# Kernel optimization log

Measured on AMD Instinct MI355X. Metric: run time of the kernel, lower is better.

The kernel has to match this reference:

```python
import jax, jax.numpy as jnp
import numpy as np

B, S, E = 2, 4096, 512

def setup_inputs() -> dict:
    key = jax.random.key(0)
    kx, kq, kk, kv, ko = jax.random.split(key, 5)
    scale = 1.0 / np.sqrt(E)  # init-style scaling for weights
    return {
        "x": jax.random.normal(kx, (B, S, E), dtype=jnp.float32),
        "Wq": jax.random.normal(kq, (E, E), dtype=jnp.float32) * scale,
        "Wk": jax.random.normal(kk, (E, E), dtype=jnp.float32) * scale,
        "Wv": jax.random.normal(kv, (E, E), dtype=jnp.float32) * scale,
        "Wo": jax.random.normal(ko, (E, E), dtype=jnp.float32) * scale,
        "bo": jnp.zeros((E,), dtype=jnp.float32),
    }

def reference(x, Wq, Wk, Wv, Wo, bo):
    # nn.Linear: y = x @ W.T  (weights stored [out, in])
    q = jnp.einsum("bse,fe->bsf", x, Wq)
    k = jnp.einsum("bse,fe->bsf", x, Wk)
    v = jnp.einsum("bse,fe->bsf", x, Wv)
    inv_scale = 1.0 / jnp.sqrt(jnp.asarray(x.shape[-1], x.dtype))
    scores = jnp.einsum("bqe,bke->bqk", q, k) * inv_scale  # [B,S,S]
    S_len = x.shape[1]
    # torch.triu(ones) keeps j >= i; masked_fill where triu==0 masks j < i
    row = jnp.arange(S_len)[:, None]
    col = jnp.arange(S_len)[None, :]
    keep = col >= row  # [S,S], faithfully anti-causal as in the source
    scores = jnp.where(keep[None, :, :], scores, jnp.asarray(-jnp.inf, scores.dtype))
    attn = jax.nn.softmax(scores, axis=-1)
    # dropout p=0.0 -> identity
    out = jnp.einsum("bqk,bke->bqe", attn, v)
    return jnp.einsum("bse,fe->bsf", out, Wo) + bo
```

## Files before the change

kernel.cpp:

```cpp
#include <hip/hip_runtime.h>
#include <hip/hip_bf16.h>

#define S_LEN 4096
#define E_DIM 512
#define B_DIM 2
#define M_ROWS (B_DIM * S_LEN)

typedef __attribute__((ext_vector_type(8))) short short8;
typedef __attribute__((ext_vector_type(4))) float floatx4;

__device__ __forceinline__ unsigned short f2bf(float f) {
    unsigned u = __float_as_uint(f);
    unsigned r = (u + 0x7fffu + ((u >> 16) & 1u)) >> 16;
    return (unsigned short)r;
}
__device__ __forceinline__ float bf2f(unsigned short u) {
    return __uint_as_float((unsigned)u << 16);
}

__device__ __forceinline__ void async_copy16(unsigned short* lds, const unsigned short* g) {
    auto gp = (const __attribute__((address_space(1))) unsigned int*)g;
    auto lp = (__attribute__((address_space(3))) unsigned int*)lds;
    __builtin_amdgcn_global_load_lds(gp, lp, 16, 0, 0);
}

struct MapArg { unsigned short m[576]; };

__global__ __launch_bounds__(256) void convert_bf16(
    const float* __restrict__ x,  const float* __restrict__ wq,
    const float* __restrict__ wk, const float* __restrict__ wv,
    const float* __restrict__ wo, unsigned short* __restrict__ dstU,
    unsigned short* __restrict__ dstWo)
{
    long i = (long)blockIdx.x * 1024 + (long)threadIdx.x * 4;
    const float* src; long off; unsigned short* dst; long doff;
    if      (i < 4194304) { src = x;  off = i;           dst = dstU;  doff = i; }
    else if (i < 4456448) { src = wq; off = i - 4194304; dst = dstU;  doff = i; }
    else if (i < 4718592) { src = wk; off = i - 4456448; dst = dstU;  doff = i; }
    else if (i < 4980736) { src = wv; off = i - 4718592; dst = dstU;  doff = i; }
    else                  { src = wo; off = i - 4980736; dst = dstWo; doff = i - 4980736; }
    float4 v = *(const float4*)(src + off);
    ushort4 o;
    o.x = f2bf(v.x); o.y = f2bf(v.y); o.z = f2bf(v.z); o.w = f2bf(v.w);
    *(ushort4*)(dst + doff) = o;
}

__device__ __forceinline__ void gemm_core(
    const unsigned short* __restrict__ A, const unsigned short* __restrict__ W,
    void* __restrict__ Cv, const float* __restrict__ bias, int mode,
    int m0, int n0)
{
    __shared__ unsigned short As[128 * 32];
    __shared__ unsigned short Bs[128 * 32];
    const int tid = threadIdx.x;
    const int lane = tid & 63, wave = tid >> 6;
    const int wm = wave >> 1, wn = wave & 1;
    const int q4 = lane >> 4, l16 = lane & 15;

    floatx4 acc[4][4];
#pragma unroll
    for (int i = 0; i < 4; ++i)
#pragma unroll
        for (int j = 0; j < 4; ++j) acc[i][j] = (floatx4){0.f, 0.f, 0.f, 0.f};

    const int srow = lane >> 2;
    const int scol = (lane & 3) * 8;

    for (int k0 = 0; k0 < 512; k0 += 32) {
        async_copy16(&As[(wave * 16) * 32],
                     A + (size_t)(m0 + wave * 16 + srow) * 512 + k0 + scol);
        async_copy16(&As[(64 + wave * 16) * 32],
                     A + (size_t)(m0 + 64 + wave * 16 + srow) * 512 + k0 + scol);
        async_copy16(&Bs[(wave * 16) * 32],
                     W + (size_t)(n0 + wave * 16 + srow) * 512 + k0 + scol);
        async_copy16(&Bs[(64 + wave * 16) * 32],
                     W + (size_t)(n0 + 64 + wave * 16 + srow) * 512 + k0 + scol);
        __syncthreads();
        short8 af[4], bfr[4];
#pragma unroll
        for (int i = 0; i < 4; ++i) {
            af[i]  = *(const short8*)&As[(wm * 64 + i * 16 + l16) * 32 + q4 * 8];
            bfr[i] = *(const short8*)&Bs[(wn * 64 + i * 16 + l16) * 32 + q4 * 8];
        }
#pragma unroll
        for (int i = 0; i < 4; ++i)
#pragma unroll
            for (int j = 0; j < 4; ++j)
                acc[i][j] = __builtin_amdgcn_mfma_f32_16x16x32_bf16(af[i], bfr[j], acc[i][j], 0, 0, 0);
        __syncthreads();
    }

    if (mode == 0) {
        unsigned short* C = (unsigned short*)Cv;
#pragma unroll
        for (int i = 0; i < 4; ++i) {
            int rowb = m0 + wm * 64 + i * 16 + q4 * 4;
#pragma unroll
            for (int j = 0; j < 4; ++j) {
                int col = n0 + wn * 64 + j * 16 + l16;
#pragma unroll
                for (int rg = 0; rg < 4; ++rg)
                    C[(size_t)(rowb + rg) * 512 + col] = f2bf(acc[i][j][rg]);
            }
        }
    } else if (mode == 1) {
        unsigned short* C = (unsigned short*)Cv;
#pragma unroll
        for (int i = 0; i < 4; ++i) {
            int grow = m0 + wm * 64 + i * 16 + q4 * 4;
            int b = grow >> 12, s = grow & 4095;
#pragma unroll
            for (int j = 0; j < 4; ++j) {
                int e = n0 + wn * 64 + j * 16 + l16;
                ushort4 pk;
                pk.x = f2bf(acc[i][j][0]); pk.y = f2bf(acc[i][j][1]);
                pk.z = f2bf(acc[i][j][2]); pk.w = f2bf(acc[i][j][3]);
                *(ushort4*)(C + (size_t)b * 512 * 4096 + (size_t)e * 4096 + s) = pk;
            }
        }
    } else {
        float* C = (float*)Cv;
#pragma unroll
        for (int i = 0; i < 4; ++i) {
            int rowb = m0 + wm * 64 + i * 16 + q4 * 4;
#pragma unroll
            for (int j = 0; j < 4; ++j) {
                int col = n0 + wn * 64 + j * 16 + l16;
                float bv = bias[col];
#pragma unroll
                for (int rg = 0; rg < 4; ++rg)
                    C[(size_t)(rowb + rg) * 512 + col] = acc[i][j][rg] + bv;
            }
        }
    }
}

__global__ __launch_bounds__(256) void gemm_qkv(
    const unsigned short* __restrict__ xb,
    const unsigned short* __restrict__ Wqb, const unsigned short* __restrict__ Wkb,
    const unsigned short* __restrict__ Wvb,
    unsigned short* __restrict__ Qb, unsigned short* __restrict__ Kb,
    unsigned short* __restrict__ Vtb)
{
    const int z = blockIdx.z;
    const unsigned short* W = (z == 0) ? Wqb : (z == 1) ? Wkb : Wvb;
    unsigned short* C = (z == 0) ? Qb : (z == 1) ? Kb : Vtb;
    gemm_core(xb, W, C, nullptr, (z == 2) ? 1 : 0, blockIdx.y * 128, blockIdx.x * 128);
}

__global__ __launch_bounds__(256) void gemm_out(
    const unsigned short* __restrict__ AOb, const unsigned short* __restrict__ Wob,
    const float* __restrict__ bo, float* __restrict__ out)
{
    gemm_core(AOb, Wob, out, bo, 2, blockIdx.y * 128, blockIdx.x * 128);
}

__global__ __launch_bounds__(512, 2) void flash_mfma(
    const unsigned short* __restrict__ Qg, const unsigned short* __restrict__ Kg,
    const unsigned short* __restrict__ Vt,
    unsigned short* __restrict__ Oh, float* __restrict__ Lb, MapArg map)
{
    const int enc = map.m[blockIdx.x];
    const int tile = enc & 63, ch = (enc >> 6) & 7, bb = enc >> 9;
    const int i0 = tile * 64;
    const int lo0 = 512 * ch, hi = lo0 + 512;
    const int lo = (i0 > lo0) ? i0 : lo0;

    const int tid = threadIdx.x;
    const int lane = tid & 63, w = tid >> 6;
    const int s = w & 3, h = w >> 2;
    const int q4 = lane >> 4, l16 = lane & 15;
    const float scale = 0.044194173824159216f;
    const float MREF = 4.0f;

    __shared__ float Sred[4][64][36];
    __shared__ unsigned short Plds[64][40];
    __shared__ float Lred[64][8];

    const size_t rowbase = (size_t)bb * S_LEN;
    const size_t vbase   = (size_t)bb * 512 * 4096;

    short8 aq[4][4];
#pragma unroll
    for (int mg = 0; mg < 4; ++mg)
#pragma unroll
        for (int ks = 0; ks < 4; ++ks)
            aq[mg][ks] = *(const short8*)(Qg + (rowbase + i0 + mg * 16 + l16) * 512
                                          + s * 128 + ks * 32 + q4 * 8);

    floatx4 oacc[4][4];
#pragma unroll
    for (int mg = 0; mg < 4; ++mg)
#pragma unroll
        for (int nc = 0; nc < 4; ++nc) oacc[mg][nc] = (floatx4){0.f, 0.f, 0.f, 0.f};

    const int r = tid >> 3;
    const int g = tid & 7;
    float l_acc = 0.f;

    auto step = [&](int j0, short8 (&bkc)[4], short8 (&bkn)[4], int jn) {
        short8 vf[4];
#pragma unroll
        for (int nc = 0; nc < 4; ++nc)
            vf[nc] = *(const short8*)(Vt + vbase
                + (size_t)(w * 64 + nc * 16 + l16) * 4096 + j0 + q4 * 8);
#pragma unroll
        for (int ks = 0; ks < 4; ++ks)
            bkn[ks] = *(const short8*)(Kg + (rowbase + jn + h * 16 + l16) * 512
                                       + s * 128 + ks * 32 + q4 * 8);
        floatx4 sf[4];
#pragma unroll
        for (int mg = 0; mg < 4; ++mg) sf[mg] = (floatx4){0.f, 0.f, 0.f, 0.f};
        __builtin_amdgcn_s_setprio(1);
#pragma unroll
        for (int ks = 0; ks < 4; ++ks)
#pragma unroll
            for (int mg = 0; mg < 4; ++mg)
                sf[mg] = __builtin_amdgcn_mfma_f32_16x16x32_bf16(
                    bkc[ks], aq[mg][ks], sf[mg], 0, 0, 0);
        __builtin_amdgcn_s_setprio(0);
#pragma unroll
        for (int mg = 0; mg < 4; ++mg)
            *(floatx4*)&Sred[s][mg * 16 + l16][h * 16 + q4 * 4] = sf[mg];
        __syncthreads();

        float4 a0 = *(const float4*)&Sred[0][r][4 * g];
        float4 a1 = *(const float4*)&Sred[1][r][4 * g];
        float4 a2 = *(const float4*)&Sred[2][r][4 * g];
        float4 a3 = *(const float4*)&Sred[3][r][4 * g];
        float sv[4] = { a0.x + a1.x + a2.x + a3.x, a0.y + a1.y + a2.y + a3.y,
                        a0.z + a1.z + a2.z + a3.z, a0.w + a1.w + a2.w + a3.w };
        ushort4 pk;
        float p0, p1, p2, p3;
        {
            int key = j0 + 4 * g;
            int row = i0 + r;
            p0 = (key + 0 >= row) ? __expf(sv[0] * scale - MREF) : 0.f;
            p1 = (key + 1 >= row) ? __expf(sv[1] * scale - MREF) : 0.f;
            p2 = (key + 2 >= row) ? __expf(sv[2] * scale - MREF) : 0.f;
            p3 = (key + 3 >= row) ? __expf(sv[3] * scale - MREF) : 0.f;
        }
        l_acc += p0 + p1 + p2 + p3;
        pk.x = f2bf(p0); pk.y = f2bf(p1); pk.z = f2bf(p2); pk.w = f2bf(p3);
        *(ushort4*)&Plds[r][4 * g] = pk;
        __syncthreads();

        short8 ap[4];
#pragma unroll
        for (int mg = 0; mg < 4; ++mg)
            ap[mg] = *(const short8*)&Plds[mg * 16 + l16][q4 * 8];
        __builtin_amdgcn_s_setprio(1);
#pragma unroll
        for (int mg = 0; mg < 4; ++mg)
#pragma unroll
            for (int nc = 0; nc < 4; ++nc)
                oacc[mg][nc] = __builtin_amdgcn_mfma_f32_16x16x32_bf16(
                    ap[mg], vf[nc], oacc[mg][nc], 0, 0, 0);
        __builtin_amdgcn_s_setprio(0);
    };

    short8 bkA[4], bkB[4];
    int j0 = hi - 32;
#pragma unroll
    for (int ks = 0; ks < 4; ++ks)
        bkA[ks] = *(const short8*)(Kg + (rowbase + j0 + h * 16 + l16) * 512
                                   + s * 128 + ks * 32 + q4 * 8);
    while (j0 >= lo) {
        int jn = (j0 - 32 >= lo) ? j0 - 32 : lo;
        step(j0, bkA, bkB, jn);
        j0 -= 32;
        if (j0 < lo) break;
        jn = (j0 - 32 >= lo) ? j0 - 32 : lo;
        step(j0, bkB, bkA, jn);
        j0 -= 32;
    }
    __syncthreads();

    const int slot = 8 * ch * (ch + 1) + bb * 8 * (ch + 1) + tile;

    Lred[r][g] = l_acc;
    __syncthreads();
    if (tid < 64) {
        float sum = 0.f;
#pragma unroll
        for (int gg = 0; gg < 8; ++gg) sum += Lred[tid][gg];
        Lb[(size_t)slot * 64 + tid] = sum;
    }

    unsigned short* Op = Oh + (size_t)slot * 64 * 512;
#pragma unroll
    for (int mg = 0; mg < 4; ++mg)
#pragma unroll
        for (int nc = 0; nc < 4; ++nc)
#pragma unroll
            for (int rg = 0; rg < 4; ++rg)
                Op[(size_t)(mg * 16 + q4 * 4 + rg) * 512 + w * 64 + nc * 16 + l16]
                    = f2bf(oacc[mg][nc][rg]);
}

__global__ __launch_bounds__(256) void flash_merge(
    const unsigned short* __restrict__ Oh, const float* __restrict__ Lb,
    unsigned short* __restrict__ AO)
{
    const int row = blockIdx.x;
    const int c = threadIdx.x * 2;
    const int bb = row >> 12, i = row & 4095;
    const int t = i >> 6, ri = i & 63;
    const int chmin = i >> 9;
    float lsum = 0.f, v0 = 0.f, v1 = 0.f;
    for (int ch = chmin; ch < 8; ++ch) {
        int slot = 8 * ch * (ch + 1) + bb * 8 * (ch + 1) + t;
        lsum += Lb[(size_t)slot * 64 + ri];
        const unsigned short* p = Oh + (size_t)slot * 64 * 512 + (size_t)ri * 512 + c;
        v0 += bf2f(p[0]);
        v1 += bf2f(p[1]);
    }
    float inv = 1.f / lsum;
    ushort2 o; o.x = f2bf(v0 * inv); o.y = f2bf(v1 * inv);
    *(ushort2*)(AO + (size_t)row * 512 + c) = o;
}

static MapArg build_map() {
    int enc[576], steps[576], n = 0;
    for (int bb = 0; bb < 2; ++bb)
        for (int ch = 0; ch < 8; ++ch)
            for (int t = 0; t < 8 * (ch + 1); ++t) {
                int i0 = t * 64, lo0 = 512 * ch, hi = lo0 + 512;
                int lo = (i0 > lo0) ? i0 : lo0;
                enc[n] = t | (ch << 6) | (bb << 9);
                steps[n] = (hi - lo) / 32;
                ++n;
            }
    static int buck[9][576];
    int bn[9] = {0};
    for (int i = 0; i < n; ++i) { int b = steps[i] >> 1; buck[b][bn[b]++] = enc[i]; }
    MapArg mp{};
    int a = 0;
    for (int c = 0; c < 16; ++c) {
        mp.m[c] = (unsigned short)buck[8][a++];
        mp.m[256 + c] = (unsigned short)buck[8][a++];
        mp.m[512 + c] = (unsigned short)buck[1][c];
    }
    for (int c = 16; c < 32; ++c) {
        mp.m[c] = (unsigned short)buck[8][a++];
        mp.m[256 + c] = (unsigned short)buck[7][c - 16];
        mp.m[512 + c] = (unsigned short)buck[2][c - 16];
    }
    for (int c = 32; c < 48; ++c) {
        mp.m[c] = (unsigned short)buck[8][a++];
        mp.m[256 + c] = (unsigned short)buck[6][c - 32];
        mp.m[512 + c] = (unsigned short)buck[3][c - 32];
    }
    for (int c = 48; c < 64; ++c) {
        mp.m[c] = (unsigned short)buck[8][a++];
        mp.m[256 + c] = (unsigned short)buck[5][c - 48];
        mp.m[512 + c] = (unsigned short)buck[4][c - 48];
    }
    for (int c = 64; c < 256; ++c) {
        mp.m[c] = (unsigned short)buck[8][a++];
        mp.m[256 + c] = (unsigned short)buck[8][a++];
    }
    return mp;
}

extern "C" void kernel_launch(void* const* d_in, const int* in_sizes, int n_in,
                              void* d_out, int out_size, void* d_ws, size_t ws_size,
                              hipStream_t stream) {
    (void)in_sizes; (void)n_in; (void)out_size; (void)ws_size;
    const float* x  = (const float*)d_in[0];
    const float* Wq = (const float*)d_in[1];
    const float* Wk = (const float*)d_in[2];
    const float* Wv = (const float*)d_in[3];
    const float* Wo = (const float*)d_in[4];
    const float* bo = (const float*)d_in[5];
    float* out = (float*)d_out;

    unsigned short* ws  = (unsigned short*)d_ws;
    unsigned short* Wob = ws;
    unsigned short* QAb = ws + 262144;
    unsigned short* Kb  = QAb + 4194304;
    unsigned short* Vtb = Kb + 4194304;
    unsigned short* U   = Vtb + 4194304;
    unsigned short* xb  = U;
    unsigned short* Wqb = U + 4194304;
    unsigned short* Wkb = Wqb + 262144;
    unsigned short* Wvb = Wkb + 262144;
    unsigned short* Ohb = U;
    float* Lbf = (float*)(U + 18874368);

    static const MapArg mp = build_map();

    convert_bf16<<<5120, 256, 0, stream>>>(x, Wq, Wk, Wv, Wo, U, Wob);

    gemm_qkv<<<dim3(4, 64, 3), 256, 0, stream>>>(xb, Wqb, Wkb, Wvb, QAb, Kb, Vtb);

    flash_mfma<<<576, 512, 0, stream>>>(QAb, Kb, Vtb, Ohb, Lbf, mp);

    flash_merge<<<8192, 256, 0, stream>>>(Ohb, Lbf, QAb);

    gemm_out<<<dim3(4, 64), 256, 0, stream>>>(QAb, Wob, bo, out);
}
```

Baseline: 233.0 us.

## Stage Q in swizzled LDS and process 128-key tiles without cross-wave score reduction

The flash kernel now stages the 64x512 Q tile into LDS with an XOR swizzle through async global-to-LDS copies, where it used to hold Q fragments in registers split across waves. Each wave computes full-depth scores for its own 16 keys of a 128-key tile, so the Sred cross-wave reduction and one barrier per step are gone. The step width goes from 32 to 128 keys, P is double-buffered, and causal masking is skipped on fully unmasked tiles. The start is aligned down to 128, which computes some masked extra work, and the block map becomes a simple longest-first ordering in place of the bucketed interleave. More LDS use and heavier register pressure from the 16 K fragments and 16 V fragments may reduce occupancy.

```diff
diff --git a/kernel.cpp b/kernel.cpp
--- a/kernel.cpp
+++ b/kernel.cpp
@@ -165,125 +165,130 @@
     const int i0 = tile * 64;
     const int lo0 = 512 * ch, hi = lo0 + 512;
     const int lo = (i0 > lo0) ? i0 : lo0;
+    const int lo_al = lo & ~127;
+    const int nsteps = (hi - lo_al) >> 7;
 
     const int tid = threadIdx.x;
     const int lane = tid & 63, w = tid >> 6;
-    const int s = w & 3, h = w >> 2;
     const int q4 = lane >> 4, l16 = lane & 15;
+    const int e = l16 & 7;
     const float scale = 0.044194173824159216f;
     const float MREF = 4.0f;
 
-    __shared__ float Sred[4][64][36];
-    __shared__ unsigned short Plds[64][40];
-    __shared__ float Lred[64][8];
+    __shared__ unsigned short Qs[64 * 512];
+    __shared__ unsigned short Plds[2][64][136];
+    __shared__ float Lred[8][64];
 
     const size_t rowbase = (size_t)bb * S_LEN;
-    const size_t vbase   = (size_t)bb * 512 * 4096;
-
-    short8 aq[4][4];
+    const size_t vbase   = (size_t)bb * (size_t)512 * 4096;
+
+#pragma unroll
+    for (int rr = 0; rr < 8; ++rr) {
+        const int row = w * 8 + rr;
+        const unsigned short* src = Qg + (rowbase + i0 + row) * 512
+                                    + ((lane ^ (row & 7)) << 3);
+        async_copy16(&Qs[row * 512], src);
+    }
+
+    floatx4 oacc[4][4];
 #pragma unroll
     for (int mg = 0; mg < 4; ++mg)
 #pragma unroll
-        for (int ks = 0; ks < 4; ++ks)
-            aq[mg][ks] = *(const short8*)(Qg + (rowbase + i0 + mg * 16 + l16) * 512
-                                          + s * 128 + ks * 32 + q4 * 8);
-
-    floatx4 oacc[4][4];
-#pragma unroll
-    for (int mg = 0; mg < 4; ++mg)
-#pragma unroll
         for (int nc = 0; nc < 4; ++nc) oacc[mg][nc] = (floatx4){0.f, 0.f, 0.f, 0.f};
-
-    const int r = tid >> 3;
-    const int g = tid & 7;
-    float l_acc = 0.f;
-
-    auto step = [&](int j0, short8 (&bkc)[4], short8 (&bkn)[4], int jn) {
-        short8 vf[4];
-#pragma unroll
-        for (int nc = 0; nc < 4; ++nc)
-            vf[nc] = *(const short8*)(Vt + vbase
-                + (size_t)(w * 64 + nc * 16 + l16) * 4096 + j0 + q4 * 8);
-#pragma unroll
-        for (int ks = 0; ks < 4; ++ks)
-            bkn[ks] = *(const short8*)(Kg + (rowbase + jn + h * 16 + l16) * 512
-                                       + s * 128 + ks * 32 + q4 * 8);
+    float l_acc[4] = {0.f, 0.f, 0.f, 0.f};
+
+    const unsigned short* qb0 = &Qs[l16 * 512 + ((q4 ^ e) << 3)];
+    const unsigned short* qb1 = &Qs[l16 * 512 + (((q4 + 4) ^ e) << 3)];
+    const unsigned short* kpbase = Kg + (rowbase + 16 * w + l16) * 512 + (q4 << 3);
+
+    __syncthreads();
+
+    for (int t = 0; t < nsteps; ++t) {
+        const int j0 = lo_al + t * 128;
+        const int buf = t & 1;
+
+        short8 kf[16];
+        const unsigned short* kp = kpbase + (size_t)j0 * 512;
+#pragma unroll
+        for (int ks = 0; ks < 16; ++ks)
+            kf[ks] = *(const short8*)(kp + ks * 32);
+
         floatx4 sf[4];
 #pragma unroll
         for (int mg = 0; mg < 4; ++mg) sf[mg] = (floatx4){0.f, 0.f, 0.f, 0.f};
         __builtin_amdgcn_s_setprio(1);
 #pragma unroll
-        for (int ks = 0; ks < 4; ++ks)
-#pragma unroll
-            for (int mg = 0; mg < 4; ++mg)
-                sf[mg] = __builtin_amdgcn_mfma_f32_16x16x32_bf16(
-                    bkc[ks], aq[mg][ks], sf[mg], 0, 0, 0);
+        for (int ks = 0; ks < 16; ++ks) {
+            const unsigned short* qb = (ks & 1) ? qb1 : qb0;
+#pragma unroll
+            for (int mg = 0; mg < 4; ++mg) {
+                short8 a = *(const short8*)(qb + mg * 8192 + (ks >> 1) * 64);
+                sf[mg] = __builtin_amdgcn_mfma_f32_16x16x32_bf16(kf[ks], a, sf[mg], 0, 0, 0);
+            }
+        }
         __builtin_amdgcn_s_setprio(0);
-#pragma unroll
-        for (int mg = 0; mg < 4; ++mg)
-            *(floatx4*)&Sred[s][mg * 16 + l16][h * 16 + q4 * 4] = sf[mg];
+
+        short8 vf[4][4];
+#pragma unroll
+        for (int nc = 0; nc < 4; ++nc) {
+            const unsigned short* vpn = Vt + vbase
+                + (size_t)(w * 64 + nc * 16 + l16) * 4096 + j0 + (q4 << 3);
+#pragma unroll
+            for (int kslot = 0; kslot < 4; ++kslot)
+                vf[nc][kslot] = *(const short8*)(vpn + kslot * 32);
+        }
+
+        const int kb = j0 + 16 * w + (q4 << 2);
+        const bool full = (j0 >= i0 + 64);
+#pragma unroll
+        for (int mg = 0; mg < 4; ++mg) {
+            const int row = i0 + mg * 16 + l16;
+            float p0 = __expf(sf[mg][0] * scale - MREF);
+            float p1 = __expf(sf[mg][1] * scale - MREF);
+            float p2 = __expf(sf[mg][2] * scale - MREF);
+            float p3 = __expf(sf[mg][3] * scale - MREF);
+            if (!full) {
+                p0 = (kb + 0 >= row) ? p0 : 0.f;
+                p1 = (kb + 1 >= row) ? p1 : 0.f;
+                p2 = (kb + 2 >= row) ? p2 : 0.f;
+                p3 = (kb + 3 >= row) ? p3 : 0.f;
+            }
+            l_acc[mg] += p0 + p1 + p2 + p3;
+            ushort4 pk;
+            pk.x = f2bf(p0); pk.y = f2bf(p1); pk.z = f2bf(p2); pk.w = f2bf(p3);
+            *(ushort4*)&Plds[buf][mg * 16 + l16][16 * w + (q4 << 2)] = pk;
+        }
         __syncthreads();
 
-        float4 a0 = *(const float4*)&Sred[0][r][4 * g];
-        float4 a1 = *(const float4*)&Sred[1][r][4 * g];
-        float4 a2 = *(const float4*)&Sred[2][r][4 * g];
-        float4 a3 = *(const float4*)&Sred[3][r][4 * g];
-        float sv[4] = { a0.x + a1.x + a2.x + a3.x, a0.y + a1.y + a2.y + a3.y,
-                        a0.z + a1.z + a2.z + a3.z, a0.w + a1.w + a2.w + a3.w };
-        ushort4 pk;
-        float p0, p1, p2, p3;
-        {
-            int key = j0 + 4 * g;
-            int row = i0 + r;
-            p0 = (key + 0 >= row) ? __expf(sv[0] * scale - MREF) : 0.f;
-            p1 = (key + 1 >= row) ? __expf(sv[1] * scale - MREF) : 0.f;
-            p2 = (key + 2 >= row) ? __expf(sv[2] * scale - MREF) : 0.f;
-            p3 = (key + 3 >= row) ? __expf(sv[3] * scale - MREF) : 0.f;
-        }
-        l_acc += p0 + p1 + p2 + p3;
-        pk.x = f2bf(p0); pk.y = f2bf(p1); pk.z = f2bf(p2); pk.w = f2bf(p3);
-        *(ushort4*)&Plds[r][4 * g] = pk;
-        __syncthreads();
-
-        short8 ap[4];
-#pragma unroll
-        for (int mg = 0; mg < 4; ++mg)
-            ap[mg] = *(const short8*)&Plds[mg * 16 + l16][q4 * 8];
         __builtin_amdgcn_s_setprio(1);
 #pragma unroll
-        for (int mg = 0; mg < 4; ++mg)
-#pragma unroll
-            for (int nc = 0; nc < 4; ++nc)
-                oacc[mg][nc] = __builtin_amdgcn_mfma_f32_16x16x32_bf16(
-                    ap[mg], vf[nc], oacc[mg][nc], 0, 0, 0);
+        for (int kslot = 0; kslot < 4; ++kslot) {
+#pragma unroll
+            for (int mg = 0; mg < 4; ++mg) {
+                short8 ap = *(const short8*)&Plds[buf][mg * 16 + l16][kslot * 32 + (q4 << 3)];
+#pragma unroll
+                for (int nc = 0; nc < 4; ++nc)
+                    oacc[mg][nc] = __builtin_amdgcn_mfma_f32_16x16x32_bf16(
+                        ap, vf[nc][kslot], oacc[mg][nc], 0, 0, 0);
+            }
+        }
         __builtin_amdgcn_s_setprio(0);
-    };
-
-    short8 bkA[4], bkB[4];
-    int j0 = hi - 32;
-#pragma unroll
-    for (int ks = 0; ks < 4; ++ks)
-        bkA[ks] = *(const short8*)(Kg + (rowbase + j0 + h * 16 + l16) * 512
-                                   + s * 128 + ks * 32 + q4 * 8);
-    while (j0 >= lo) {
-        int jn = (j0 - 32 >= lo) ? j0 - 32 : lo;
-        step(j0, bkA, bkB, jn);
-        j0 -= 32;
-        if (j0 < lo) break;
-        jn = (j0 - 32 >= lo) ? j0 - 32 : lo;
-        step(j0, bkB, bkA, jn);
-        j0 -= 32;
+    }
+
+#pragma unroll
+    for (int mg = 0; mg < 4; ++mg) {
+        float v = l_acc[mg];
+        v += __shfl_xor(v, 16, 64);
+        v += __shfl_xor(v, 32, 64);
+        if (q4 == 0) Lred[w][mg * 16 + l16] = v;
     }
     __syncthreads();
 
     const int slot = 8 * ch * (ch + 1) + bb * 8 * (ch + 1) + tile;
-
-    Lred[r][g] = l_acc;
-    __syncthreads();
     if (tid < 64) {
         float sum = 0.f;
 #pragma unroll
-        for (int gg = 0; gg < 8; ++gg) sum += Lred[tid][gg];
+        for (int ww = 0; ww < 8; ++ww) sum += Lred[ww][tid];
         Lb[(size_t)slot * 64 + tid] = sum;
     }
 
@@ -327,39 +332,16 @@
             for (int t = 0; t < 8 * (ch + 1); ++t) {
                 int i0 = t * 64, lo0 = 512 * ch, hi = lo0 + 512;
                 int lo = (i0 > lo0) ? i0 : lo0;
+                int lo_al = lo & ~127;
                 enc[n] = t | (ch << 6) | (bb << 9);
-                steps[n] = (hi - lo) / 32;
+                steps[n] = (hi - lo_al) >> 7;
                 ++n;
             }
-    static int buck[9][576];
-    int bn[9] = {0};
-    for (int i = 0; i < n; ++i) { int b = steps[i] >> 1; buck[b][bn[b]++] = enc[i]; }
     MapArg mp{};
-    int a = 0;
-    for (int c = 0; c < 16; ++c) {
-        mp.m[c] = (unsigned short)buck[8][a++];
-        mp.m[256 + c] = (unsigned short)buck[8][a++];
-        mp.m[512 + c] = (unsigned short)buck[1][c];
-    }
-    for (int c = 16; c < 32; ++c) {
-        mp.m[c] = (unsigned short)buck[8][a++];
-        mp.m[256 + c] = (unsigned short)buck[7][c - 16];
-        mp.m[512 + c] = (unsigned short)buck[2][c - 16];
-    }
-    for (int c = 32; c < 48; ++c) {
-        mp.m[c] = (unsigned short)buck[8][a++];
-        mp.m[256 + c] = (unsigned short)buck[6][c - 32];
-        mp.m[512 + c] = (unsigned short)buck[3][c - 32];
-    }
-    for (int c = 48; c < 64; ++c) {
-        mp.m[c] = (unsigned short)buck[8][a++];
-        mp.m[256 + c] = (unsigned short)buck[5][c - 48];
-        mp.m[512 + c] = (unsigned short)buck[4][c - 48];
-    }
-    for (int c = 64; c < 256; ++c) {
-        mp.m[c] = (unsigned short)buck[8][a++];
-        mp.m[256 + c] = (unsigned short)buck[8][a++];
-    }
+    int idx = 0;
+    for (int sv = 4; sv >= 1; --sv)
+        for (int i = 0; i < n; ++i)
+            if (steps[i] == sv) mp.m[idx++] = (unsigned short)enc[i];
     return mp;
 }
 
```

Result: faster. 215.5 us (-7.5%).
